# Optimization experiments

Measured on AMD Instinct MI355X. Metric: run time of the kernel, lower is better.

The kernel has to match this reference:

```python
import jax, jax.numpy as jnp
import numpy as np

K = 32
NEG = 0.2


def _knn_idx(pts, k):
    # pts: [B,N,C]. Negative squared pairwise distance; top-k = k nearest (incl. self).
    xx = jnp.sum(pts * pts, axis=-1)                      # [B,N]
    inner = jnp.einsum('bnc,bmc->bnm', pts, pts)          # [B,N,N]
    d = 2.0 * inner - xx[:, :, None] - xx[:, None, :]
    return jax.lax.top_k(d, k)[1]                         # [B,N,K]


def _edge_conv(pts, W, s, b, k=K):
    # pts: [B,N,C] -> [B,N,O]. EdgeConv: gather knn, (nbr-ctr, ctr) feature,
    # 1x1 conv (matmul) + folded-BN affine + LeakyReLU, max over k.
    idx = _knn_idx(pts, k)
    nbr = jax.vmap(lambda p, i: p[i])(pts, idx)           # [B,N,K,C]
    ctr = jnp.broadcast_to(pts[:, :, None, :], nbr.shape)
    feat = jnp.concatenate([nbr - ctr, ctr], axis=-1)     # [B,N,K,2C]
    h = jnp.einsum('bnkc,oc->bnko', feat, W)
    h = jax.nn.leaky_relu(h * s + b, NEG)
    return jnp.max(h, axis=2)                             # [B,N,O]


def reference(x, W1, s1, b1, W2, s2, b2, W3, s3, b3, W4, s4, b4, W5, s5, b5,
              L1w, s6, b6, L2w, L2b, s7, b7, L3w, L3b,
              F1w, s8, b8, F2w, F2b, s9, b9, F3w, F3b):
    pts = jnp.transpose(x, (0, 2, 1))                     # [B,N,3]
    x1 = _edge_conv(pts, W1, s1, b1)                      # [B,N,64]
    x2 = _edge_conv(x1, W2, s2, b2)                       # [B,N,64]
    x3 = _edge_conv(x2, W3, s3, b3)                       # [B,N,128]
    x4 = _edge_conv(x3, W4, s4, b4)                       # [B,N,256]
    cat = jnp.concatenate([x1, x2, x3, x4], axis=-1)      # [B,N,512]
    h = jnp.einsum('bnc,oc->bno', cat, W5)                # [B,N,1024]
    h = jax.nn.leaky_relu(h * s5 + b5, NEG)
    # y branch: global max pool -> fc1/bn8 -> fc2/bn9 -> fc3 (dropout=identity, eval)
    y = jnp.max(h, axis=1)                                # [B,1024]
    y = jax.nn.leaky_relu((y @ F1w.T) * s8 + b8, NEG)
    y = jax.nn.leaky_relu((y @ F2w.T + F2b) * s9 + b9, NEG)
    y = y @ F3w.T + F3b                                   # [B,5]
    # x branch: max+avg pool -> linear1/bn6 -> linear2/bn7 -> linear3
    g = jnp.concatenate([jnp.max(h, axis=1), jnp.mean(h, axis=1)], axis=-1)  # [B,2048]
    g = jax.nn.leaky_relu((g @ L1w.T) * s6 + b6, NEG)
    g = jax.nn.leaky_relu((g @ L2w.T + L2b) * s7 + b7, NEG)
    g = g @ L3w.T + L3b                                   # [B,5]
    return (g, y)


def setup_inputs():
    key = jax.random.key(0)
    ks = iter(jax.random.split(key, 64))

    def rn(shape, scale=1.0):
        return jax.random.normal(next(ks), shape, dtype=jnp.float32) * scale

    B, N = 8, 2048
    d = {"x": rn((B, 3, N))}

    def bn(n, c):  # folded inference BN: scale (positive) and bias
        d["s" + n] = jnp.abs(rn((c,), 0.1)) + 1.0
        d["b" + n] = rn((c,), 0.1)

    d["W1"] = rn((64, 6), 0.1); bn("1", 64)
    d["W2"] = rn((64, 128), 0.1); bn("2", 64)
    d["W3"] = rn((128, 128), 0.1); bn("3", 128)
    d["W4"] = rn((256, 256), 0.05); bn("4", 256)
    d["W5"] = rn((1024, 512), 0.05); bn("5", 1024)
    d["L1w"] = rn((512, 2048), 0.02); bn("6", 512)
    d["L2w"] = rn((256, 512), 0.05); d["L2b"] = rn((256,), 0.1); bn("7", 256)
    d["L3w"] = rn((5, 256), 0.1); d["L3b"] = rn((5,), 0.1)
    d["F1w"] = rn((512, 1024), 0.02); bn("8", 512)
    d["F2w"] = rn((256, 512), 0.05); d["F2b"] = rn((256,), 0.1); bn("9", 256)
    d["F3w"] = rn((5, 256), 0.1); d["F3b"] = rn((5,), 0.1)
    return d
```

## Files before the change

kernel.cpp:

```cpp
#include <hip/hip_runtime.h>
#include <math.h>

constexpr int Bn = 8;
constexpr int Np = 2048;
constexpr int Kn = 32;
constexpr float NEGS = 0.2f;

typedef __attribute__((ext_vector_type(8))) short short8;
typedef __attribute__((ext_vector_type(4))) float f32x4;
typedef unsigned short ushortT;

__device__ __forceinline__ float lrelu(float v) { return v > 0.f ? v : NEGS * v; }

template<int CTRL, int RMASK>
__device__ __forceinline__ float dppmax(float v) {
    int o = __float_as_int(v);
    int s = __builtin_amdgcn_update_dpp(o, o, CTRL, RMASK, 0xf, false);
    return fmaxf(v, __int_as_float(s));
}
__device__ __forceinline__ float wave_max_dpp(float v) {
    v = dppmax<0x111, 0xf>(v);
    v = dppmax<0x112, 0xf>(v);
    v = dppmax<0x114, 0xf>(v);
    v = dppmax<0x118, 0xf>(v);
    v = dppmax<0x142, 0xa>(v);
    v = dppmax<0x143, 0xc>(v);
    return __int_as_float(__builtin_amdgcn_readlane(__float_as_int(v), 63));
}

__device__ __forceinline__ void cvt2u(float a, float b, unsigned& h, unsigned& l) {
    unsigned ua = __float_as_uint(a), ub = __float_as_uint(b);
    h = (ua >> 16) | (ub & 0xffff0000u);
    float ra = a - __uint_as_float(ua & 0xffff0000u);
    float rb = b - __uint_as_float(ub & 0xffff0000u);
    l = (__float_as_uint(ra) >> 16) | (__float_as_uint(rb) & 0xffff0000u);
}

__global__ __launch_bounds__(256) void k_transpose(const float* __restrict__ x, float* __restrict__ pts) {
    int i = blockIdx.x * 256 + threadIdx.x;
    int b = i / Np, n = i % Np;
    float p0 = x[((size_t)b * 3 + 0) * Np + n];
    float p1 = x[((size_t)b * 3 + 1) * Np + n];
    float p2 = x[((size_t)b * 3 + 2) * Np + n];
    float4 v = make_float4(p0, p1, p2, 0.f);
    *(float4*)&pts[(size_t)i * 4] = v;
}

__global__ __launch_bounds__(256) void k_xx(const float* __restrict__ pm, float* __restrict__ xxg, int C, int ld) {
    int wid = threadIdx.x >> 6, lane = threadIdx.x & 63;
    int pt = blockIdx.x * 4 + wid;
    const float* row = pm + (size_t)pt * ld;
    float acc = 0.f;
    for (int c = lane; c < C; c += 64) { float v = row[c]; acc = fmaf(v, v, acc); }
    #pragma unroll
    for (int off = 32; off; off >>= 1) acc += __shfl_down(acc, off, 64);
    if (lane == 0) xxg[pt] = acc;
}

template<int C, int CK, int LD>
__global__ __launch_bounds__(256) void k_bpack(const float* __restrict__ Xpm,
                                               ushortT* __restrict__ Bh, ushortT* __restrict__ Bl) {
    constexpr int KS = CK / 32;
    int i = blockIdx.x * 256 + threadIdx.x;
    int j = i & 7;
    int lane = (i >> 3) & 63;
    int nt = (i >> 9) & 127;
    int rest = i >> 16;
    int ks = rest % KS;
    int b = rest / KS;
    int k = ks * 32 + (lane >> 4) * 8 + j;
    int n = nt * 16 + (lane & 15);
    float v = (k < C) ? Xpm[((size_t)b * Np + n) * LD + k] : 0.f;
    unsigned u = __float_as_uint(v);
    Bh[i] = (ushortT)(u >> 16);
    float r = v - __uint_as_float(u & 0xffff0000u);
    Bl[i] = (ushortT)(__float_as_uint(r) >> 16);
}

template<int CC, int KS, int CPv, int SDv>
__device__ __forceinline__ void dist_compute(
    const ushortT* __restrict__ Ah, const ushortT* __restrict__ Al,
    float* __restrict__ dl, const float* __restrict__ xxg,
    const ushortT* __restrict__ Bh, const ushortT* __restrict__ Bl,
    int b, int w, int lane, int quad, int col,
    const float (&xmr)[4])
{
    short8 ah[KS], al[KS];
    #pragma unroll
    for (int ks = 0; ks < KS; ++ks) {
        ah[ks] = *(const short8*)&Ah[col * CPv + ks * 32 + quad * 8];
        al[ks] = *(const short8*)&Al[col * CPv + ks * 32 + quad * 8];
    }
    #pragma unroll
    for (int i = 0; i < 2; ++i) {
        int ntl0 = w * 4 + 2 * i, ntl1 = ntl0 + 1;
        int ng0 = CC * 64 + ntl0, ng1 = CC * 64 + ntl1;
        f32x4 a0 = (f32x4){0.f, 0.f, 0.f, 0.f};
        f32x4 a1 = (f32x4){0.f, 0.f, 0.f, 0.f};
        #pragma unroll
        for (int ks = 0; ks < KS; ++ks) {
            int bi0 = (((b * KS + ks) * 128 + ng0) * 64 + lane) * 8;
            int bi1 = (((b * KS + ks) * 128 + ng1) * 64 + lane) * 8;
            short8 bh0 = *(const short8*)(Bh + bi0);
            short8 bl0 = *(const short8*)(Bl + bi0);
            short8 bh1 = *(const short8*)(Bh + bi1);
            short8 bl1 = *(const short8*)(Bl + bi1);
            a0 = __builtin_amdgcn_mfma_f32_16x16x32_bf16(ah[ks], bh0, a0, 0, 0, 0);
            a1 = __builtin_amdgcn_mfma_f32_16x16x32_bf16(ah[ks], bh1, a1, 0, 0, 0);
            a0 = __builtin_amdgcn_mfma_f32_16x16x32_bf16(ah[ks], bl0, a0, 0, 0, 0);
            a1 = __builtin_amdgcn_mfma_f32_16x16x32_bf16(ah[ks], bl1, a1, 0, 0, 0);
            a0 = __builtin_amdgcn_mfma_f32_16x16x32_bf16(al[ks], bh0, a0, 0, 0, 0);
            a1 = __builtin_amdgcn_mfma_f32_16x16x32_bf16(al[ks], bh1, a1, 0, 0, 0);
        }
        float xn0 = xxg[b * Np + ng0 * 16 + col];
        float xn1 = xxg[b * Np + ng1 * 16 + col];
        #pragma unroll
        for (int r = 0; r < 4; ++r) {
            int m = quad * 4 + r;
            dl[m * SDv + ntl0 * 16 + col] = 2.f * a0[r] - xmr[r] - xn0;
            dl[m * SDv + ntl1 * 16 + col] = 2.f * a1[r] - xmr[r] - xn1;
        }
    }
}

template<int C, int CK, int LD>
__global__ __launch_bounds__(1024) void k_knn5(const float* __restrict__ Xpm,
                                               const ushortT* __restrict__ Bh, const ushortT* __restrict__ Bl,
                                               const float* __restrict__ xxg, int* __restrict__ idxo) {
    constexpr int KS = CK / 32, CP = CK + 8, CK4 = CK / 4, C4src = LD / 4;
    constexpr int SD = 1026;
    extern __shared__ char smem[];
    ushortT* Ah = (ushortT*)smem;
    ushortT* Al = Ah + 16 * CP;
    float* xxm = (float*)(Al + 16 * CP);
    float* dl = xxm + 16;
    int nwg = gridDim.x;
    int cpx = nwg >> 3;
    int logical = (blockIdx.x & 7) * cpx + (blockIdx.x >> 3);
    int b = logical / (Np / 16);
    int n0 = (logical % (Np / 16)) * 16;
    int t = threadIdx.x;
    const float4* Xp4 = (const float4*)Xpm;
    for (int e = t; e < 16 * CK4; e += 1024) {
        int r = e / CK4, c4 = e % CK4;
        float4 v = (c4 < C4src) ? Xp4[((size_t)b * Np + n0 + r) * C4src + c4] : make_float4(0.f, 0.f, 0.f, 0.f);
        unsigned h0, l0, h1, l1;
        cvt2u(v.x, v.y, h0, l0);
        cvt2u(v.z, v.w, h1, l1);
        *(uint2*)&Ah[r * CP + 4 * c4] = make_uint2(h0, h1);
        *(uint2*)&Al[r * CP + 4 * c4] = make_uint2(l0, l1);
    }
    if (t < 16) xxm[t] = xxg[b * Np + t + n0];
    __syncthreads();

    int w = t >> 6, lane = t & 63;
    int quad = lane >> 4, col = lane & 15;
    float xmr[4];
    #pragma unroll
    for (int r = 0; r < 4; ++r) xmr[r] = xxm[quad * 4 + r];

    const float* drow = dl + w * SD;
    float v0, v1, v2, v3, v4, v5, v6, v7, v8, v9, v10, v11, v12, v13, v14, v15;
    float v16, v17, v18, v19, v20, v21, v22, v23, v24, v25, v26, v27, v28, v29, v30, v31;

    dist_compute<0, KS, CP, SD>(Ah, Al, dl, xxg, Bh, Bl, b, w, lane, quad, col, xmr);
    __syncthreads();
    v0  = drow[lane +  0 * 64]; v1  = drow[lane +  1 * 64];
    v2  = drow[lane +  2 * 64]; v3  = drow[lane +  3 * 64];
    v4  = drow[lane +  4 * 64]; v5  = drow[lane +  5 * 64];
    v6  = drow[lane +  6 * 64]; v7  = drow[lane +  7 * 64];
    v8  = drow[lane +  8 * 64]; v9  = drow[lane +  9 * 64];
    v10 = drow[lane + 10 * 64]; v11 = drow[lane + 11 * 64];
    v12 = drow[lane + 12 * 64]; v13 = drow[lane + 13 * 64];
    v14 = drow[lane + 14 * 64]; v15 = drow[lane + 15 * 64];
    __syncthreads();
    dist_compute<1, KS, CP, SD>(Ah, Al, dl, xxg, Bh, Bl, b, w, lane, quad, col, xmr);
    __syncthreads();
    v16 = drow[lane +  0 * 64]; v17 = drow[lane +  1 * 64];
    v18 = drow[lane +  2 * 64]; v19 = drow[lane +  3 * 64];
    v20 = drow[lane +  4 * 64]; v21 = drow[lane +  5 * 64];
    v22 = drow[lane +  6 * 64]; v23 = drow[lane +  7 * 64];
    v24 = drow[lane +  8 * 64]; v25 = drow[lane +  9 * 64];
    v26 = drow[lane + 10 * 64]; v27 = drow[lane + 11 * 64];
    v28 = drow[lane + 12 * 64]; v29 = drow[lane + 13 * 64];
    v30 = drow[lane + 14 * 64]; v31 = drow[lane + 15 * 64];

    float s0v = -INFINITY, s1v = -INFINITY, s2v = -INFINITY, s3v = -INFINITY;
    int s0i = 0, s1i = 0, s2i = 0, s3i = 0;

#define INS4(VV, JJ) { \
    bool b0 = (VV) > s0v, b1 = (VV) > s1v, b2 = (VV) > s2v, b3 = (VV) > s3v; \
    s3v = b2 ? s2v : (b3 ? (VV) : s3v);  s3i = b2 ? s2i : (b3 ? (JJ) : s3i); \
    s2v = b1 ? s1v : (b2 ? (VV) : s2v);  s2i = b1 ? s1i : (b2 ? (JJ) : s2i); \
    s1v = b0 ? s0v : (b1 ? (VV) : s1v);  s1i = b0 ? s0i : (b1 ? (JJ) : s1i); \
    s0v = b0 ? (VV) : s0v;               s0i = b0 ? (JJ) : s0i; \
}
    INS4(v0, 0)   INS4(v1, 1)   INS4(v2, 2)   INS4(v3, 3)
    INS4(v4, 4)   INS4(v5, 5)   INS4(v6, 6)   INS4(v7, 7)
    INS4(v8, 8)   INS4(v9, 9)   INS4(v10, 10) INS4(v11, 11)
    INS4(v12, 12) INS4(v13, 13) INS4(v14, 14) INS4(v15, 15)
    INS4(v16, 16) INS4(v17, 17) INS4(v18, 18) INS4(v19, 19)
    INS4(v20, 20) INS4(v21, 21) INS4(v22, 22) INS4(v23, 23)
    INS4(v24, 24) INS4(v25, 25) INS4(v26, 26) INS4(v27, 27)
    INS4(v28, 28) INS4(v29, 29) INS4(v30, 30) INS4(v31, 31)

    unsigned umask = 0u;
    int pops = 0;
    size_t ob = ((size_t)b * Np + n0 + w) * Kn;
    for (int it = 0; it < Kn; ++it) {
        float Wv = wave_max_dpp(s0v);
        unsigned long long mk = __ballot(s0v == Wv);
        int owner = __ffsll(mk) - 1;
        bool pred = (lane == owner);
        if (pred) idxo[ob + it] = lane + (s0i << 6);
        umask |= pred ? (1u << s0i) : 0u;
        pops = pred ? (pops + 1) : pops;
        s0v = pred ? s1v : s0v;  s0i = pred ? s1i : s0i;
        s1v = pred ? s2v : s1v;  s1i = pred ? s2i : s1i;
        s2v = pred ? s3v : s2v;  s2i = pred ? s3i : s2i;
        s3v = pred ? -INFINITY : s3v;
        bool need = pred && (pops >= 4);
        if (__ballot(need)) {
            if (need) {
                pops = 0;
                s0v = s1v = s2v = s3v = -INFINITY;
                s0i = s1i = s2i = s3i = 0;
#define RINS(VV, JJ) { float vv_ = ((umask >> (JJ)) & 1u) ? -INFINITY : (VV); INS4(vv_, JJ) }
                RINS(v0, 0)   RINS(v1, 1)   RINS(v2, 2)   RINS(v3, 3)
                RINS(v4, 4)   RINS(v5, 5)   RINS(v6, 6)   RINS(v7, 7)
                RINS(v8, 8)   RINS(v9, 9)   RINS(v10, 10) RINS(v11, 11)
                RINS(v12, 12) RINS(v13, 13) RINS(v14, 14) RINS(v15, 15)
                RINS(v16, 16) RINS(v17, 17) RINS(v18, 18) RINS(v19, 19)
                RINS(v20, 20) RINS(v21, 21) RINS(v22, 22) RINS(v23, 23)
                RINS(v24, 24) RINS(v25, 25) RINS(v26, 26) RINS(v27, 27)
                RINS(v28, 28) RINS(v29, 29) RINS(v30, 30) RINS(v31, 31)
#undef RINS
            }
        }
    }
#undef INS4
}

__global__ __launch_bounds__(256) void k_wsplit(const float* __restrict__ W, const float* __restrict__ s,
                                                int C, int O, float* __restrict__ WnsT, float* __restrict__ WdsT) {
    int i = blockIdx.x * 256 + threadIdx.x;
    if (i >= C * O) return;
    int c = i / O, o = i % O;
    float a = W[(size_t)o * 2 * C + c];
    float q = W[(size_t)o * 2 * C + C + c];
    float sv = s[o];
    WnsT[i] = a * sv;
    WdsT[i] = (q - a) * sv;
}

__global__ __launch_bounds__(256) void k_wpack(const float* __restrict__ W, const float* __restrict__ s,
                                               int C, int O, ushortT* __restrict__ Bh, ushortT* __restrict__ Bl) {
    int i = blockIdx.x * 256 + threadIdx.x;
    if (i >= C * O) return;
    int k = i / O, o = i % O;
    float v = W[(size_t)o * 2 * C + k] * s[o];
    int ks = k >> 5, quad = (k >> 3) & 3, j = k & 7;
    int nt = o >> 4, lane = quad * 16 + (o & 15);
    int NT = O / 16;
    size_t idx = (((size_t)(ks * NT + nt)) * 64 + lane) * 8 + j;
    unsigned u = __float_as_uint(v);
    Bh[idx] = (ushortT)(u >> 16);
    float r = v - __uint_as_float(u & 0xffff0000u);
    Bl[idx] = (ushortT)(__float_as_uint(r) >> 16);
}

__global__ __launch_bounds__(256) void k_w5pack(const float* __restrict__ W5, const float* __restrict__ s5,
                                                ushortT* __restrict__ Bh, ushortT* __restrict__ Bl) {
    int i = blockIdx.x * 256 + threadIdx.x;
    int k = i >> 10, o = i & 1023;
    float v = W5[(size_t)o * 512 + k] * s5[o];
    int ks = k >> 5, quad = (k >> 3) & 3, j = k & 7;
    int nt = o >> 4, lane = quad * 16 + (o & 15);
    size_t idx = (((size_t)(ks * 64 + nt)) * 64 + lane) * 8 + j;
    unsigned u = __float_as_uint(v);
    Bh[idx] = (ushortT)(u >> 16);
    float r = v - __uint_as_float(u & 0xffff0000u);
    Bl[idx] = (ushortT)(__float_as_uint(r) >> 16);
}

template<int C, int O, int OPT>
__global__ __launch_bounds__(256) void k_ctr(const float* __restrict__ Xpm, const float* __restrict__ WdsT,
                                             const float* __restrict__ bg, float* __restrict__ cb) {
    constexpr int OG = O / OPT, MG = 256 / OG, MPT = 32 / MG;
    constexpr int C4 = C / 4;
    __shared__ float xs[32][C];
    int b = blockIdx.x / (Np / 32);
    int n0 = (blockIdx.x % (Np / 32)) * 32;
    int t = threadIdx.x;
    const float4* Xp4 = (const float4*)Xpm;
    for (int e = t; e < 32 * C4; e += 256) {
        int pt = e / C4, c4 = e % C4;
        *(float4*)&xs[pt][4 * c4] = Xp4[((size_t)b * Np + n0 + pt) * C4 + c4];
    }
    __syncthreads();
    int og = t % OG, mg = t / OG;
    int o0 = og * OPT;
    float acc[MPT][OPT] = {};
    for (int c = 0; c < C; ++c) {
        float wv[OPT];
        #pragma unroll
        for (int p4 = 0; p4 < OPT / 4; ++p4)
            *(float4*)&wv[4 * p4] = *(const float4*)&WdsT[(size_t)c * O + o0 + 4 * p4];
        #pragma unroll
        for (int m = 0; m < MPT; ++m) {
            float xv = xs[mg * MPT + m][c];
            #pragma unroll
            for (int p = 0; p < OPT; ++p) acc[m][p] = fmaf(wv[p], xv, acc[m][p]);
        }
    }
    #pragma unroll
    for (int m = 0; m < MPT; ++m) {
        #pragma unroll
        for (int p = 0; p < OPT; ++p) {
            int o = o0 + p;
            cb[((size_t)b * Np + n0 + mg * MPT + m) * O + o] = acc[m][p] + bg[o];
        }
    }
}

template<int C, int O, int PTS>
__global__ __launch_bounds__(256, 4) void k_ec3(const float* __restrict__ Xpm, const int* __restrict__ idxg,
                                                const ushortT* __restrict__ Bh, const ushortT* __restrict__ Bl,
                                                const float* __restrict__ cb,
                                                float* __restrict__ Ypm) {
    static_assert(PTS == 2, "M=64 mapping");
    constexpr int M = 64, NT = O / 16, NT4 = NT / 4, KS = C / 32, C4 = C / 4, CP = C + 8;
    static_assert(NT4 >= 1, "O>=64");
    __shared__ ushortT Ah[M][CP];
    __shared__ ushortT Al[M][CP];
    int b = blockIdx.x / (Np / PTS);
    int n0 = (blockIdx.x % (Np / PTS)) * PTS;
    int t = threadIdx.x;
    const int* ip = idxg + ((size_t)b * Np + n0) * Kn;
    const float4* Xp4 = (const float4*)Xpm;
    for (int e = t; e < M * C4; e += 256) {
        int row = e / C4, c4 = e % C4;
        float4 v = Xp4[((size_t)b * Np + ip[row]) * C4 + c4];
        unsigned h0, l0, h1, l1;
        cvt2u(v.x, v.y, h0, l0);
        cvt2u(v.z, v.w, h1, l1);
        *(uint2*)&Ah[row][4 * c4] = make_uint2(h0, h1);
        *(uint2*)&Al[row][4 * c4] = make_uint2(l0, l1);
    }
    __syncthreads();
    int w = t >> 6, lane = t & 63;
    int quad = lane >> 4, col = lane & 15;
    f32x4 acc[4][NT4];
    #pragma unroll
    for (int mt = 0; mt < 4; ++mt)
        #pragma unroll
        for (int i = 0; i < NT4; ++i) acc[mt][i] = (f32x4){0.f, 0.f, 0.f, 0.f};
    for (int ks = 0; ks < KS; ++ks) {
        int kb = ks * 32 + quad * 8;
        short8 ah[4], al[4];
        #pragma unroll
        for (int mt = 0; mt < 4; ++mt) {
            ah[mt] = *(const short8*)&Ah[mt * 16 + col][kb];
            al[mt] = *(const short8*)&Al[mt * 16 + col][kb];
        }
        #pragma unroll
        for (int i = 0; i < NT4; ++i) {
            int nt = w * NT4 + i;
            size_t bi = (((size_t)(ks * NT + nt)) * 64 + lane) * 8;
            short8 bh = *(const short8*)(Bh + bi);
            short8 bl = *(const short8*)(Bl + bi);
            #pragma unroll
            for (int mt = 0; mt < 4; ++mt) {
                acc[mt][i] = __builtin_amdgcn_mfma_f32_16x16x32_bf16(ah[mt], bh, acc[mt][i], 0, 0, 0);
                acc[mt][i] = __builtin_amdgcn_mfma_f32_16x16x32_bf16(ah[mt], bl, acc[mt][i], 0, 0, 0);
                acc[mt][i] = __builtin_amdgcn_mfma_f32_16x16x32_bf16(al[mt], bh, acc[mt][i], 0, 0, 0);
            }
        }
    }
    #pragma unroll
    for (int pt = 0; pt < PTS; ++pt) {
        size_t ni = (size_t)b * Np + n0 + pt;
        #pragma unroll
        for (int i = 0; i < NT4; ++i) {
            f32x4 a0 = acc[2 * pt][i], a1 = acc[2 * pt + 1][i];
            float m = fmaxf(fmaxf(fmaxf(a0[0], a0[1]), fmaxf(a0[2], a0[3])),
                            fmaxf(fmaxf(a1[0], a1[1]), fmaxf(a1[2], a1[3])));
            m = fmaxf(m, __shfl_xor(m, 16, 64));
            m = fmaxf(m, __shfl_xor(m, 32, 64));
            if (lane < 16) {
                int o = (w * NT4 + i) * 16 + col;
                Ypm[ni * O + o] = lrelu(m + cb[ni * O + o]);
            }
        }
    }
}

template<int C, int CPAD, int O, int OPT, int KPT, int PTS>
__global__ __launch_bounds__(256) void k_edgeconv(
    const float* __restrict__ Xpm, const int* __restrict__ idxg,
    const float* __restrict__ W, const float* __restrict__ sg, const float* __restrict__ bg,
    float* __restrict__ Ypm)
{
    constexpr int OG = O / OPT;
    constexpr int NKG = 256 / OG;
    constexpr int CL = CPAD + 4;
    static_assert(NKG * KPT == Kn, "k mapping");
    __shared__ float nbr[PTS][Kn][CL];
    __shared__ float ctr[PTS][CPAD];
    __shared__ float red[PTS][OPT][4][OG];
    int blk = blockIdx.x;
    int b = blk / (Np / PTS);
    int n0 = (blk % (Np / PTS)) * PTS;
    int t = threadIdx.x;
    int lane = t & 63, wid = t >> 6;
    const int* ip = idxg + ((size_t)b * Np + n0) * Kn;
    const float4* Xp4 = (const float4*)Xpm;
    constexpr int C4 = CPAD / 4;
    for (int e = t; e < PTS * C4; e += 256) {
        int pt = e / C4, c4 = e % C4;
        *(float4*)&ctr[pt][4 * c4] = Xp4[((size_t)b * Np + n0 + pt) * C4 + c4];
    }
    for (int e = t; e < PTS * Kn * C4; e += 256) {
        int pt = e / (Kn * C4);
        int r = e % (Kn * C4);
        int k = r / C4, c4 = r % C4;
        int nb = ip[pt * Kn + k];
        *(float4*)&nbr[pt][k][4 * c4] = Xp4[((size_t)b * Np + nb) * C4 + c4];
    }
    __syncthreads();
    int og = t % OG, kg = t / OG;
    float acc[PTS][OPT][KPT] = {};
    float ctt[PTS][OPT] = {};
    for (int c0 = 0; c0 < CPAD; c0 += 4) {
        float wn[OPT][4], wd[OPT][4];
        #pragma unroll
        for (int p = 0; p < OPT; ++p) {
            #pragma unroll
            for (int cc = 0; cc < 4; ++cc) {
                int c = c0 + cc;
                float a = (c < C) ? W[(size_t)(og + p * OG) * (2 * C) + c] : 0.f;
                float q = (c < C) ? W[(size_t)(og + p * OG) * (2 * C) + C + c] : 0.f;
                wn[p][cc] = a; wd[p][cc] = q - a;
            }
        }
        #pragma unroll
        for (int pt = 0; pt < PTS; ++pt) {
            float4 cv = *(const float4*)&ctr[pt][c0];
            #pragma unroll
            for (int p = 0; p < OPT; ++p) {
                ctt[pt][p] = fmaf(wd[p][0], cv.x, ctt[pt][p]);
                ctt[pt][p] = fmaf(wd[p][1], cv.y, ctt[pt][p]);
                ctt[pt][p] = fmaf(wd[p][2], cv.z, ctt[pt][p]);
                ctt[pt][p] = fmaf(wd[p][3], cv.w, ctt[pt][p]);
            }
        }
        #pragma unroll
        for (int pt = 0; pt < PTS; ++pt) {
            #pragma unroll
            for (int k = 0; k < KPT; ++k) {
                float4 nv = *(const float4*)&nbr[pt][kg * KPT + k][c0];
                #pragma unroll
                for (int p = 0; p < OPT; ++p) {
                    acc[pt][p][k] = fmaf(wn[p][0], nv.x, acc[pt][p][k]);
                    acc[pt][p][k] = fmaf(wn[p][1], nv.y, acc[pt][p][k]);
                    acc[pt][p][k] = fmaf(wn[p][2], nv.z, acc[pt][p][k]);
                    acc[pt][p][k] = fmaf(wn[p][3], nv.w, acc[pt][p][k]);
                }
            }
        }
    }
    #pragma unroll
    for (int pt = 0; pt < PTS; ++pt) {
        #pragma unroll
        for (int p = 0; p < OPT; ++p) {
            int o = og + p * OG;
            float sv = sg[o], bv = bg[o];
            float m = -INFINITY;
            #pragma unroll
            for (int k = 0; k < KPT; ++k) {
                float hv = fmaf(acc[pt][p][k] + ctt[pt][p], sv, bv);
                m = fmaxf(m, lrelu(hv));
            }
            #pragma unroll
            for (int s = OG; s < 64; s <<= 1) m = fmaxf(m, __shfl_xor(m, s, 64));
            if (lane < OG) red[pt][p][wid][lane] = m;
        }
    }
    __syncthreads();
    if (t < OG) {
        #pragma unroll
        for (int pt = 0; pt < PTS; ++pt) {
            #pragma unroll
            for (int p = 0; p < OPT; ++p) {
                float m = fmaxf(fmaxf(red[pt][p][0][t], red[pt][p][1][t]),
                                fmaxf(red[pt][p][2][t], red[pt][p][3][t]));
                int o = t + p * OG;
                Ypm[((size_t)b * Np + n0 + pt) * O + o] = m;
            }
        }
    }
}

__global__ __launch_bounds__(1024, 4) void k_w5mfma(
    const float* __restrict__ x1, const float* __restrict__ x2,
    const float* __restrict__ x3, const float* __restrict__ x4,
    const ushortT* __restrict__ Bh, const ushortT* __restrict__ Bl,
    const float* __restrict__ b5,
    float* __restrict__ pmax, float* __restrict__ psum)
{
    constexpr int CP = 520;
    extern __shared__ char smem[];
    ushortT* Ah = (ushortT*)smem;
    ushortT* Al = Ah + 32 * CP;
    int b = blockIdx.x >> 6;
    int chunk = blockIdx.x & 63;
    int n0 = chunk * 32;
    int t = threadIdx.x;
    for (int e = t; e < 32 * 128; e += 1024) {
        int pt = e >> 7, c4 = e & 127;
        size_t pi = (size_t)b * Np + n0 + pt;
        float4 v;
        if (c4 < 16)      v = ((const float4*)x1)[pi * 16 + c4];
        else if (c4 < 32) v = ((const float4*)x2)[pi * 16 + (c4 - 16)];
        else if (c4 < 64) v = ((const float4*)x3)[pi * 32 + (c4 - 32)];
        else              v = ((const float4*)x4)[pi * 64 + (c4 - 64)];
        unsigned h0, l0, h1, l1;
        cvt2u(v.x, v.y, h0, l0);
        cvt2u(v.z, v.w, h1, l1);
        *(uint2*)&Ah[pt * CP + 4 * c4] = make_uint2(h0, h1);
        *(uint2*)&Al[pt * CP + 4 * c4] = make_uint2(l0, l1);
    }
    __syncthreads();
    int w = t >> 6, lane = t & 63;
    int quad = lane >> 4, col = lane & 15;
    size_t pb = ((size_t)(b * 64 + chunk)) * 1024;
    for (int oi = 0; oi < 4; ++oi) {
        int nt = w * 4 + oi;
        f32x4 a0 = (f32x4){0.f, 0.f, 0.f, 0.f};
        f32x4 a1 = (f32x4){0.f, 0.f, 0.f, 0.f};
        #pragma unroll 2
        for (int ks = 0; ks < 16; ++ks) {
            size_t bi = (((size_t)(ks * 64 + nt)) * 64 + lane) * 8;
            short8 bh = *(const short8*)(Bh + bi);
            short8 bl = *(const short8*)(Bl + bi);
            int ao = ks * 32 + quad * 8;
            short8 ah0 = *(const short8*)&Ah[col * CP + ao];
            short8 al0 = *(const short8*)&Al[col * CP + ao];
            short8 ah1 = *(const short8*)&Ah[(16 + col) * CP + ao];
            short8 al1 = *(const short8*)&Al[(16 + col) * CP + ao];
            a0 = __builtin_amdgcn_mfma_f32_16x16x32_bf16(ah0, bh, a0, 0, 0, 0);
            a1 = __builtin_amdgcn_mfma_f32_16x16x32_bf16(ah1, bh, a1, 0, 0, 0);
            a0 = __builtin_amdgcn_mfma_f32_16x16x32_bf16(ah0, bl, a0, 0, 0, 0);
            a1 = __builtin_amdgcn_mfma_f32_16x16x32_bf16(ah1, bl, a1, 0, 0, 0);
            a0 = __builtin_amdgcn_mfma_f32_16x16x32_bf16(al0, bh, a0, 0, 0, 0);
            a1 = __builtin_amdgcn_mfma_f32_16x16x32_bf16(al1, bh, a1, 0, 0, 0);
        }
        float bb = b5[nt * 16 + col];
        float mx = -INFINITY, sm = 0.f;
        #pragma unroll
        for (int r = 0; r < 4; ++r) {
            float v0 = lrelu(a0[r] + bb);
            float v1 = lrelu(a1[r] + bb);
            mx = fmaxf(mx, fmaxf(v0, v1));
            sm += v0 + v1;
        }
        mx = fmaxf(mx, __shfl_xor(mx, 16, 64));
        mx = fmaxf(mx, __shfl_xor(mx, 32, 64));
        sm += __shfl_xor(sm, 16, 64);
        sm += __shfl_xor(sm, 32, 64);
        if (lane < 16) {
            pmax[pb + nt * 16 + col] = mx;
            psum[pb + nt * 16 + col] = sm;
        }
    }
}

__global__ __launch_bounds__(256) void k_poolred(const float* __restrict__ pmax, const float* __restrict__ psum,
                                                 float* __restrict__ g0) {
    int i = blockIdx.x * 256 + threadIdx.x;
    int b = i >> 10, o = i & 1023;
    float mx = -INFINITY, sm = 0.f;
    for (int ch = 0; ch < 64; ++ch) {
        size_t idx = ((size_t)(b * 64 + ch)) * 1024 + o;
        mx = fmaxf(mx, pmax[idx]);
        sm += psum[idx];
    }
    g0[(size_t)b * 2048 + o] = mx;
    g0[(size_t)b * 2048 + 1024 + o] = sm * (1.f / Np);
}

__global__ __launch_bounds__(256) void k_fc(const float* __restrict__ In, int ldIn, int C,
                                            const float* __restrict__ Wm,
                                            const float* __restrict__ bias,
                                            const float* __restrict__ sc, const float* __restrict__ bnb,
                                            int leaky, float* __restrict__ Out, int ldOut, int O) {
    int wid = threadIdx.x >> 6, lane = threadIdx.x & 63;
    int o = blockIdx.x * 4 + wid;
    int b = blockIdx.y;
    if (o >= O) return;
    const float* in = In + (size_t)b * ldIn;
    const float* wr = Wm + (size_t)o * C;
    float acc = 0.f;
    for (int c = lane; c < C; c += 64) acc = fmaf(in[c], wr[c], acc);
    #pragma unroll
    for (int off = 32; off; off >>= 1) acc += __shfl_down(acc, off, 64);
    if (lane == 0) {
        float v = acc + (bias ? bias[o] : 0.f);
        if (sc) v = fmaf(v, sc[o], bnb[o]);
        if (leaky) v = lrelu(v);
        Out[(size_t)b * ldOut + o] = v;
    }
}

extern "C" void kernel_launch(void* const* d_in, const int* in_sizes, int n_in,
                              void* d_out, int out_size, void* d_ws, size_t ws_size,
                              hipStream_t stream) {
    const float* x   = (const float*)d_in[0];
    const float* W1  = (const float*)d_in[1];
    const float* s1  = (const float*)d_in[2];
    const float* b1  = (const float*)d_in[3];
    const float* W2  = (const float*)d_in[4];
    const float* s2  = (const float*)d_in[5];
    const float* b2  = (const float*)d_in[6];
    const float* W3  = (const float*)d_in[7];
    const float* s3  = (const float*)d_in[8];
    const float* b3  = (const float*)d_in[9];
    const float* W4  = (const float*)d_in[10];
    const float* s4  = (const float*)d_in[11];
    const float* b4  = (const float*)d_in[12];
    const float* W5  = (const float*)d_in[13];
    const float* s5  = (const float*)d_in[14];
    const float* b5  = (const float*)d_in[15];
    const float* L1w = (const float*)d_in[16];
    const float* s6  = (const float*)d_in[17];
    const float* b6  = (const float*)d_in[18];
    const float* L2w = (const float*)d_in[19];
    const float* L2b = (const float*)d_in[20];
    const float* s7  = (const float*)d_in[21];
    const float* b7  = (const float*)d_in[22];
    const float* L3w = (const float*)d_in[23];
    const float* L3b = (const float*)d_in[24];
    const float* F1w = (const float*)d_in[25];
    const float* s8  = (const float*)d_in[26];
    const float* b8  = (const float*)d_in[27];
    const float* F2w = (const float*)d_in[28];
    const float* F2b = (const float*)d_in[29];
    const float* s9  = (const float*)d_in[30];
    const float* b9  = (const float*)d_in[31];
    const float* F3w = (const float*)d_in[32];
    const float* F3b = (const float*)d_in[33];

    float* ws = (float*)d_ws;
    size_t off = 0;
    auto alloc = [&](size_t n) { float* p = ws + off; off += n; return p; };
    float* pts  = alloc((size_t)Bn * Np * 4);
    float* x1   = alloc((size_t)Bn * Np * 64);
    float* x2   = alloc((size_t)Bn * Np * 64);
    float* x3   = alloc((size_t)Bn * Np * 128);
    float* x4   = alloc((size_t)Bn * Np * 256);
    float* xcm  = alloc((size_t)Bn * Np * 128);
    float* xxb  = alloc((size_t)Bn * Np);
    int*   idxb = (int*)alloc((size_t)Bn * Np * Kn);
    float* g0   = alloc((size_t)Bn * 2048);
    float* g1   = alloc((size_t)Bn * 512);
    float* g2   = alloc((size_t)Bn * 256);
    float* y1   = alloc((size_t)Bn * 512);
    float* y2   = alloc((size_t)Bn * 256);
    float* WnsT2 = alloc(64 * 64);
    float* WdsT2 = alloc(64 * 64);
    float* WnsT3 = alloc(64 * 128);
    float* WdsT3 = alloc(64 * 128);
    float* WnsT4 = alloc(128 * 256);
    float* WdsT4 = alloc(128 * 256);
    ushortT* Bh2 = (ushortT*)alloc(64 * 64 / 2);
    ushortT* Bl2 = (ushortT*)alloc(64 * 64 / 2);
    ushortT* Bh3 = (ushortT*)alloc(64 * 128 / 2);
    ushortT* Bl3 = (ushortT*)alloc(64 * 128 / 2);
    ushortT* Bh4 = (ushortT*)alloc(128 * 256 / 2);
    ushortT* Bl4 = (ushortT*)alloc(128 * 256 / 2);
    ushortT* BhK = (ushortT*)alloc(1048576);
    ushortT* BlK = (ushortT*)alloc(1048576);
    ushortT* Bh5 = (ushortT*)alloc(262144);
    ushortT* Bl5 = (ushortT*)alloc(262144);
    float* pmax = xcm;
    float* psum = xcm + 524288;
    float* cb2 = x2;
    float* cb3 = x3;
    float* cb4 = x4;

    auto shsz = [](int CP) { return 16 * CP * 2 * 2 + 64 + 16 * 1026 * 4; };
    int sh3 = shsz(40), sh64 = shsz(72), sh128 = shsz(136);
    int shw5 = 32 * 520 * 2 * 2;
    (void)hipFuncSetAttribute((const void*)k_knn5<3, 32, 4>, hipFuncAttributeMaxDynamicSharedMemorySize, sh3);
    (void)hipFuncSetAttribute((const void*)k_knn5<64, 64, 64>, hipFuncAttributeMaxDynamicSharedMemorySize, sh64);
    (void)hipFuncSetAttribute((const void*)k_knn5<128, 128, 128>, hipFuncAttributeMaxDynamicSharedMemorySize, sh128);
    (void)hipFuncSetAttribute((const void*)k_w5mfma, hipFuncAttributeMaxDynamicSharedMemorySize, shw5);

    k_transpose<<<Bn * Np / 256, 256, 0, stream>>>(x, pts);
    k_wsplit<<<16, 256, 0, stream>>>(W2, s2, 64, 64, WnsT2, WdsT2);
    k_wsplit<<<32, 256, 0, stream>>>(W3, s3, 64, 128, WnsT3, WdsT3);
    k_wsplit<<<128, 256, 0, stream>>>(W4, s4, 128, 256, WnsT4, WdsT4);
    k_wpack<<<16, 256, 0, stream>>>(W2, s2, 64, 64, Bh2, Bl2);
    k_wpack<<<32, 256, 0, stream>>>(W3, s3, 64, 128, Bh3, Bl3);
    k_wpack<<<128, 256, 0, stream>>>(W4, s4, 128, 256, Bh4, Bl4);
    k_w5pack<<<2048, 256, 0, stream>>>(W5, s5, Bh5, Bl5);

    k_xx<<<Bn * Np / 4, 256, 0, stream>>>(pts, xxb, 3, 4);
    k_bpack<3, 32, 4><<<2048, 256, 0, stream>>>(pts, BhK, BlK);
    k_knn5<3, 32, 4><<<Bn * Np / 16, 1024, sh3, stream>>>(pts, BhK, BlK, xxb, idxb);
    k_edgeconv<3, 4, 64, 1, 8, 4><<<Bn * Np / 4, 256, 0, stream>>>(pts, idxb, W1, s1, b1, x1);

    k_xx<<<Bn * Np / 4, 256, 0, stream>>>(x1, xxb, 64, 64);
    k_bpack<64, 64, 64><<<4096, 256, 0, stream>>>(x1, BhK, BlK);
    k_knn5<64, 64, 64><<<Bn * Np / 16, 1024, sh64, stream>>>(x1, BhK, BlK, xxb, idxb);
    k_ctr<64, 64, 4><<<Bn * Np / 32, 256, 0, stream>>>(x1, WdsT2, b2, cb2);
    k_ec3<64, 64, 2><<<Bn * Np / 2, 256, 0, stream>>>(x1, idxb, Bh2, Bl2, cb2, x2);

    k_xx<<<Bn * Np / 4, 256, 0, stream>>>(x2, xxb, 64, 64);
    k_bpack<64, 64, 64><<<4096, 256, 0, stream>>>(x2, BhK, BlK);
    k_knn5<64, 64, 64><<<Bn * Np / 16, 1024, sh64, stream>>>(x2, BhK, BlK, xxb, idxb);
    k_ctr<64, 128, 8><<<Bn * Np / 32, 256, 0, stream>>>(x2, WdsT3, b3, cb3);
    k_ec3<64, 128, 2><<<Bn * Np / 2, 256, 0, stream>>>(x2, idxb, Bh3, Bl3, cb3, x3);

    k_xx<<<Bn * Np / 4, 256, 0, stream>>>(x3, xxb, 128, 128);
    k_bpack<128, 128, 128><<<8192, 256, 0, stream>>>(x3, BhK, BlK);
    k_knn5<128, 128, 128><<<Bn * Np / 16, 1024, sh128, stream>>>(x3, BhK, BlK, xxb, idxb);
    k_ctr<128, 256, 8><<<Bn * Np / 32, 256, 0, stream>>>(x3, WdsT4, b4, cb4);
    k_ec3<128, 256, 2><<<Bn * Np / 2, 256, 0, stream>>>(x3, idxb, Bh4, Bl4, cb4, x4);

    k_w5mfma<<<Bn * 64, 1024, shw5, stream>>>(x1, x2, x3, x4, Bh5, Bl5, b5, pmax, psum);
    k_poolred<<<Bn * 1024 / 256, 256, 0, stream>>>(pmax, psum, g0);

    float* out = (float*)d_out;
    k_fc<<<dim3(128, Bn), 256, 0, stream>>>(g0, 2048, 2048, L1w, nullptr, s6, b6, 1, g1, 512, 512);
    k_fc<<<dim3(64, Bn), 256, 0, stream>>>(g1, 512, 512, L2w, L2b, s7, b7, 1, g2, 256, 256);
    k_fc<<<dim3(2, Bn), 256, 0, stream>>>(g2, 256, 256, L3w, L3b, nullptr, nullptr, 0, out, 5, 5);
    k_fc<<<dim3(128, Bn), 256, 0, stream>>>(g0, 2048, 1024, F1w, nullptr, s8, b8, 1, y1, 512, 512);
    k_fc<<<dim3(64, Bn), 256, 0, stream>>>(y1, 512, 512, F2w, F2b, s9, b9, 1, y2, 256, 256);
    k_fc<<<dim3(2, Bn), 256, 0, stream>>>(y2, 256, 256, F3w, F3b, nullptr, nullptr, 0, out + 40, 5, 5);
}
```

Baseline: 849.1 us.

## Store gathered neighbor tile in MFMA fragment order and prefetch B fragments

```diff
diff --git a/kernel.cpp b/kernel.cpp
--- a/kernel.cpp
+++ b/kernel.cpp
@@ -329,67 +329,89 @@
                                                 const float* __restrict__ cb,
                                                 float* __restrict__ Ypm) {
     static_assert(PTS == 2, "M=64 mapping");
-    constexpr int M = 64, NT = O / 16, NT4 = NT / 4, KS = C / 32, C4 = C / 4, CP = C + 8;
+    constexpr int M = 64, NT = O / 16, NT4 = NT / 4, KS = C / 32, C4 = C / 4;
+    constexpr int IH = (NT4 > 2) ? 2 : 1, IW = NT4 / IH;
     static_assert(NT4 >= 1, "O>=64");
-    __shared__ ushortT Ah[M][CP];
-    __shared__ ushortT Al[M][CP];
+    __shared__ ushortT AhF[M * C];
+    __shared__ ushortT AlF[M * C];
     int b = blockIdx.x / (Np / PTS);
     int n0 = (blockIdx.x % (Np / PTS)) * PTS;
     int t = threadIdx.x;
+    int w = t >> 6, lane = t & 63;
+    int quad = lane >> 4, col = lane & 15;
     const int* ip = idxg + ((size_t)b * Np + n0) * Kn;
     const float4* Xp4 = (const float4*)Xpm;
-    for (int e = t; e < M * C4; e += 256) {
-        int row = e / C4, c4 = e % C4;
-        float4 v = Xp4[((size_t)b * Np + ip[row]) * C4 + c4];
-        unsigned h0, l0, h1, l1;
-        cvt2u(v.x, v.y, h0, l0);
-        cvt2u(v.z, v.w, h1, l1);
-        *(uint2*)&Ah[row][4 * c4] = make_uint2(h0, h1);
-        *(uint2*)&Al[row][4 * c4] = make_uint2(l0, l1);
-    }
-    __syncthreads();
-    int w = t >> 6, lane = t & 63;
-    int quad = lane >> 4, col = lane & 15;
-    f32x4 acc[4][NT4];
-    #pragma unroll
-    for (int mt = 0; mt < 4; ++mt)
-        #pragma unroll
-        for (int i = 0; i < NT4; ++i) acc[mt][i] = (f32x4){0.f, 0.f, 0.f, 0.f};
+
+    int grow = ip[w * 16 + col];
+    size_t gbase = ((size_t)b * Np + grow) * C4;
+    #pragma unroll
     for (int ks = 0; ks < KS; ++ks) {
-        int kb = ks * 32 + quad * 8;
-        short8 ah[4], al[4];
-        #pragma unroll
-        for (int mt = 0; mt < 4; ++mt) {
-            ah[mt] = *(const short8*)&Ah[mt * 16 + col][kb];
-            al[mt] = *(const short8*)&Al[mt * 16 + col][kb];
-        }
-        #pragma unroll
-        for (int i = 0; i < NT4; ++i) {
-            int nt = w * NT4 + i;
-            size_t bi = (((size_t)(ks * NT + nt)) * 64 + lane) * 8;
-            short8 bh = *(const short8*)(Bh + bi);
-            short8 bl = *(const short8*)(Bl + bi);
+        int c4a = (ks * 32 + quad * 8) >> 2;
+        float4 va = Xp4[gbase + c4a];
+        float4 vb = Xp4[gbase + c4a + 1];
+        unsigned h0, l0, h1, l1, h2, l2, h3, l3;
+        cvt2u(va.x, va.y, h0, l0);
+        cvt2u(va.z, va.w, h1, l1);
+        cvt2u(vb.x, vb.y, h2, l2);
+        cvt2u(vb.z, vb.w, h3, l3);
+        int fo = ((w * KS + ks) * 64 + lane) * 8;
+        *(uint4*)&AhF[fo] = make_uint4(h0, h1, h2, h3);
+        *(uint4*)&AlF[fo] = make_uint4(l0, l1, l2, l3);
+    }
+    __syncthreads();
+
+    #pragma unroll
+    for (int ih = 0; ih < IH; ++ih) {
+        f32x4 acc[4][IW];
+        #pragma unroll
+        for (int mt = 0; mt < 4; ++mt)
+            #pragma unroll
+            for (int iw = 0; iw < IW; ++iw) acc[mt][iw] = (f32x4){0.f, 0.f, 0.f, 0.f};
+
+        size_t b00 = (((size_t)(0 * NT + w * NT4 + ih * IW)) * 64 + lane) * 8;
+        short8 nbh = *(const short8*)(Bh + b00);
+        short8 nbl = *(const short8*)(Bl + b00);
+        #pragma unroll
+        for (int ks = 0; ks < KS; ++ks) {
+            short8 ah[4], al[4];
             #pragma unroll
             for (int mt = 0; mt < 4; ++mt) {
-                acc[mt][i] = __builtin_amdgcn_mfma_f32_16x16x32_bf16(ah[mt], bh, acc[mt][i], 0, 0, 0);
-                acc[mt][i] = __builtin_amdgcn_mfma_f32_16x16x32_bf16(ah[mt], bl, acc[mt][i], 0, 0, 0);
-                acc[mt][i] = __builtin_amdgcn_mfma_f32_16x16x32_bf16(al[mt], bh, acc[mt][i], 0, 0, 0);
-            }
-        }
-    }
-    #pragma unroll
-    for (int pt = 0; pt < PTS; ++pt) {
-        size_t ni = (size_t)b * Np + n0 + pt;
-        #pragma unroll
-        for (int i = 0; i < NT4; ++i) {
-            f32x4 a0 = acc[2 * pt][i], a1 = acc[2 * pt + 1][i];
-            float m = fmaxf(fmaxf(fmaxf(a0[0], a0[1]), fmaxf(a0[2], a0[3])),
-                            fmaxf(fmaxf(a1[0], a1[1]), fmaxf(a1[2], a1[3])));
-            m = fmaxf(m, __shfl_xor(m, 16, 64));
-            m = fmaxf(m, __shfl_xor(m, 32, 64));
-            if (lane < 16) {
-                int o = (w * NT4 + i) * 16 + col;
-                Ypm[ni * O + o] = lrelu(m + cb[ni * O + o]);
+                int fo = ((mt * KS + ks) * 64 + lane) * 8;
+                ah[mt] = *(const short8*)&AhF[fo];
+                al[mt] = *(const short8*)&AlF[fo];
+            }
+            #pragma unroll
+            for (int iw = 0; iw < IW; ++iw) {
+                short8 bh = nbh, bl = nbl;
+                if (!(ks == KS - 1 && iw == IW - 1)) {
+                    int nks = (iw == IW - 1) ? ks + 1 : ks;
+                    int niw = (iw == IW - 1) ? 0 : iw + 1;
+                    size_t bi = (((size_t)(nks * NT + w * NT4 + ih * IW + niw)) * 64 + lane) * 8;
+                    nbh = *(const short8*)(Bh + bi);
+                    nbl = *(const short8*)(Bl + bi);
+                }
+                #pragma unroll
+                for (int mt = 0; mt < 4; ++mt) {
+                    acc[mt][iw] = __builtin_amdgcn_mfma_f32_16x16x32_bf16(ah[mt], bh, acc[mt][iw], 0, 0, 0);
+                    acc[mt][iw] = __builtin_amdgcn_mfma_f32_16x16x32_bf16(ah[mt], bl, acc[mt][iw], 0, 0, 0);
+                    acc[mt][iw] = __builtin_amdgcn_mfma_f32_16x16x32_bf16(al[mt], bh, acc[mt][iw], 0, 0, 0);
+                }
+            }
+        }
+        #pragma unroll
+        for (int pt = 0; pt < PTS; ++pt) {
+            size_t ni = (size_t)b * Np + n0 + pt;
+            #pragma unroll
+            for (int iw = 0; iw < IW; ++iw) {
+                f32x4 a0 = acc[2 * pt][iw], a1 = acc[2 * pt + 1][iw];
+                float m = fmaxf(fmaxf(fmaxf(a0[0], a0[1]), fmaxf(a0[2], a0[3])),
+                                fmaxf(fmaxf(a1[0], a1[1]), fmaxf(a1[2], a1[3])));
+                m = fmaxf(m, __shfl_xor(m, 16, 64));
+                m = fmaxf(m, __shfl_xor(m, 32, 64));
+                if (lane < 16) {
+                    int o = (w * NT4 + ih * IW + iw) * 16 + col;
+                    Ypm[ni * O + o] = lrelu(m + cb[ni * O + o]);
+                }
             }
         }
     }
```

Result: faster. 827.8 us (-2.5%).

## Read gathered edge-conv operands directly from packed kNN bf16 buffers

Applied to the files above, without the earlier changes.

```diff
diff --git a/kernel.cpp b/kernel.cpp
--- a/kernel.cpp
+++ b/kernel.cpp
@@ -324,59 +324,63 @@
 }
 
 template<int C, int O, int PTS>
-__global__ __launch_bounds__(256, 4) void k_ec3(const float* __restrict__ Xpm, const int* __restrict__ idxg,
+__global__ __launch_bounds__(256, 3) void k_ec3(const ushortT* __restrict__ Agh, const ushortT* __restrict__ Agl,
+                                                const int* __restrict__ idxg,
                                                 const ushortT* __restrict__ Bh, const ushortT* __restrict__ Bl,
                                                 const float* __restrict__ cb,
                                                 float* __restrict__ Ypm) {
     static_assert(PTS == 2, "M=64 mapping");
-    constexpr int M = 64, NT = O / 16, NT4 = NT / 4, KS = C / 32, C4 = C / 4, CP = C + 8;
+    constexpr int NT = O / 16, NT4 = NT / 4, KS = C / 32;
+    constexpr int NTT = Np / 16;
+    constexpr int KSTRIDE = NTT * 64 * 8;
     static_assert(NT4 >= 1, "O>=64");
-    __shared__ ushortT Ah[M][CP];
-    __shared__ ushortT Al[M][CP];
     int b = blockIdx.x / (Np / PTS);
     int n0 = (blockIdx.x % (Np / PTS)) * PTS;
     int t = threadIdx.x;
-    const int* ip = idxg + ((size_t)b * Np + n0) * Kn;
-    const float4* Xp4 = (const float4*)Xpm;
-    for (int e = t; e < M * C4; e += 256) {
-        int row = e / C4, c4 = e % C4;
-        float4 v = Xp4[((size_t)b * Np + ip[row]) * C4 + c4];
-        unsigned h0, l0, h1, l1;
-        cvt2u(v.x, v.y, h0, l0);
-        cvt2u(v.z, v.w, h1, l1);
-        *(uint2*)&Ah[row][4 * c4] = make_uint2(h0, h1);
-        *(uint2*)&Al[row][4 * c4] = make_uint2(l0, l1);
-    }
-    __syncthreads();
     int w = t >> 6, lane = t & 63;
     int quad = lane >> 4, col = lane & 15;
+    const int* ip = idxg + ((size_t)b * Np + n0) * Kn;
+
+    int aoff[4];
+    #pragma unroll
+    for (int mt = 0; mt < 4; ++mt) {
+        int n = ip[mt * 16 + col];
+        aoff[mt] = (((b * KS) * NTT + (n >> 4)) * 64 + quad * 16 + (n & 15)) * 8;
+    }
+
     f32x4 acc[4][NT4];
     #pragma unroll
     for (int mt = 0; mt < 4; ++mt)
         #pragma unroll
         for (int i = 0; i < NT4; ++i) acc[mt][i] = (f32x4){0.f, 0.f, 0.f, 0.f};
+
+    #pragma unroll
     for (int ks = 0; ks < KS; ++ks) {
-        int kb = ks * 32 + quad * 8;
         short8 ah[4], al[4];
         #pragma unroll
         for (int mt = 0; mt < 4; ++mt) {
-            ah[mt] = *(const short8*)&Ah[mt * 16 + col][kb];
-            al[mt] = *(const short8*)&Al[mt * 16 + col][kb];
-        }
+            int fo = aoff[mt] + ks * KSTRIDE;
+            ah[mt] = *(const short8*)(Agh + fo);
+            al[mt] = *(const short8*)(Agl + fo);
+        }
+        short8 bh[NT4], bl[NT4];
         #pragma unroll
         for (int i = 0; i < NT4; ++i) {
-            int nt = w * NT4 + i;
-            size_t bi = (((size_t)(ks * NT + nt)) * 64 + lane) * 8;
-            short8 bh = *(const short8*)(Bh + bi);
-            short8 bl = *(const short8*)(Bl + bi);
+            size_t bi = (((size_t)(ks * NT + w * NT4 + i)) * 64 + lane) * 8;
+            bh[i] = *(const short8*)(Bh + bi);
+            bl[i] = *(const short8*)(Bl + bi);
+        }
+        #pragma unroll
+        for (int i = 0; i < NT4; ++i) {
             #pragma unroll
             for (int mt = 0; mt < 4; ++mt) {
-                acc[mt][i] = __builtin_amdgcn_mfma_f32_16x16x32_bf16(ah[mt], bh, acc[mt][i], 0, 0, 0);
-                acc[mt][i] = __builtin_amdgcn_mfma_f32_16x16x32_bf16(ah[mt], bl, acc[mt][i], 0, 0, 0);
-                acc[mt][i] = __builtin_amdgcn_mfma_f32_16x16x32_bf16(al[mt], bh, acc[mt][i], 0, 0, 0);
+                acc[mt][i] = __builtin_amdgcn_mfma_f32_16x16x32_bf16(ah[mt], bh[i], acc[mt][i], 0, 0, 0);
+                acc[mt][i] = __builtin_amdgcn_mfma_f32_16x16x32_bf16(ah[mt], bl[i], acc[mt][i], 0, 0, 0);
+                acc[mt][i] = __builtin_amdgcn_mfma_f32_16x16x32_bf16(al[mt], bh[i], acc[mt][i], 0, 0, 0);
             }
         }
     }
+
     #pragma unroll
     for (int pt = 0; pt < PTS; ++pt) {
         size_t ni = (size_t)b * Np + n0 + pt;
@@ -714,19 +718,19 @@
     k_bpack<64, 64, 64><<<4096, 256, 0, stream>>>(x1, BhK, BlK);
     k_knn5<64, 64, 64><<<Bn * Np / 16, 1024, sh64, stream>>>(x1, BhK, BlK, xxb, idxb);
     k_ctr<64, 64, 4><<<Bn * Np / 32, 256, 0, stream>>>(x1, WdsT2, b2, cb2);
-    k_ec3<64, 64, 2><<<Bn * Np / 2, 256, 0, stream>>>(x1, idxb, Bh2, Bl2, cb2, x2);
+    k_ec3<64, 64, 2><<<Bn * Np / 2, 256, 0, stream>>>(BhK, BlK, idxb, Bh2, Bl2, cb2, x2);
 
     k_xx<<<Bn * Np / 4, 256, 0, stream>>>(x2, xxb, 64, 64);
     k_bpack<64, 64, 64><<<4096, 256, 0, stream>>>(x2, BhK, BlK);
     k_knn5<64, 64, 64><<<Bn * Np / 16, 1024, sh64, stream>>>(x2, BhK, BlK, xxb, idxb);
     k_ctr<64, 128, 8><<<Bn * Np / 32, 256, 0, stream>>>(x2, WdsT3, b3, cb3);
-    k_ec3<64, 128, 2><<<Bn * Np / 2, 256, 0, stream>>>(x2, idxb, Bh3, Bl3, cb3, x3);
+    k_ec3<64, 128, 2><<<Bn * Np / 2, 256, 0, stream>>>(BhK, BlK, idxb, Bh3, Bl3, cb3, x3);
 
     k_xx<<<Bn * Np / 4, 256, 0, stream>>>(x3, xxb, 128, 128);
     k_bpack<128, 128, 128><<<8192, 256, 0, stream>>>(x3, BhK, BlK);
     k_knn5<128, 128, 128><<<Bn * Np / 16, 1024, sh128, stream>>>(x3, BhK, BlK, xxb, idxb);
     k_ctr<128, 256, 8><<<Bn * Np / 32, 256, 0, stream>>>(x3, WdsT4, b4, cb4);
-    k_ec3<128, 256, 2><<<Bn * Np / 2, 256, 0, stream>>>(x3, idxb, Bh4, Bl4, cb4, x4);
+    k_ec3<128, 256, 2><<<Bn * Np / 2, 256, 0, stream>>>(BhK, BlK, idxb, Bh4, Bl4, cb4, x4);
 
     k_w5mfma<<<Bn * 64, 1024, shw5, stream>>>(x1, x2, x3, x4, Bh5, Bl5, b5, pmax, psum);
     k_poolred<<<Bn * 1024 / 256, 256, 0, stream>>>(pmax, psum, g0);
```

New measurement: 1.049 ms. 23.5% more time.
